# Performance work log

Measured on AMD Instinct MI355X. Metric: run time of the kernel, lower is better.

## Reference

```python
import jax, jax.numpy as jnp
import numpy as np
from jax import lax

B, S, N, C = 8, 256, 64, 64  # batch, time=freq (square, required by concat), n, c
EPS = 1e-3  # keras BatchNormalization / LayerNormalization default epsilon


def _conv(x, w, b):
    # 3x3 stride-1 SAME conv, NHWC / HWIO
    return lax.conv_general_dilated(x, w, (1, 1), 'SAME',
                                    dimension_numbers=('NHWC', 'HWIO', 'NHWC')) + b


def _bn(x, g, b):
    # training-mode batch norm: stats over batch+spatial axes
    m = jnp.mean(x, (0, 1, 2))
    v = jnp.var(x, (0, 1, 2))
    return (x - m) * lax.rsqrt(v + EPS) * g + b


def _ln(x, g, b):
    m = jnp.mean(x, -1, keepdims=True)
    v = jnp.var(x, -1, keepdims=True)
    return (x - m) * lax.rsqrt(v + EPS) * g + b


def _attn(q, k, v):
    # q,k,v: [B, C, L, D]; scaled dot-product attention over axis L
    d = q.shape[-1]
    s = jnp.einsum('bcid,bcjd->bcij', q, k) / jnp.sqrt(jnp.float32(d))
    a = jax.nn.softmax(s, axis=-1)
    return jnp.einsum('bcij,bcjd->bcid', a, v)


def setup_inputs():
    key = jax.random.key(0)
    ks = jax.random.split(key, 16)
    w = lambda k, sh: jax.random.normal(k, sh, jnp.float32) * 0.05
    inp = {
        'inputs': jax.random.normal(ks[0], (B, S, S, N), jnp.float32),
        'wq': w(ks[1], (3, 3, N, C)), 'bq': jnp.zeros((C,), jnp.float32),
        'wk': w(ks[2], (3, 3, N, C)), 'bk': jnp.zeros((C,), jnp.float32),
        'wv': w(ks[3], (3, 3, N, C)), 'bv': jnp.zeros((C,), jnp.float32),
        'gq': jnp.ones((C,), jnp.float32), 'betaq': jnp.zeros((C,), jnp.float32),
        'gk': jnp.ones((C,), jnp.float32), 'betak': jnp.zeros((C,), jnp.float32),
        'gv': jnp.ones((C,), jnp.float32), 'betav': jnp.zeros((C,), jnp.float32),
        'wc': w(ks[4], (3, 3, 2 * S, N)), 'bc': jnp.zeros((N,), jnp.float32),
        'ln_g': jnp.ones((N,), jnp.float32), 'ln_b': jnp.zeros((N,), jnp.float32),
        'w1': w(ks[5], (3, 3, N, N)), 'b1': jnp.zeros((N,), jnp.float32),
        'g1': jnp.ones((N,), jnp.float32), 'beta1': jnp.zeros((N,), jnp.float32),
        'w2': w(ks[6], (3, 3, N, N)), 'b2': jnp.zeros((N,), jnp.float32),
        'g2': jnp.ones((N,), jnp.float32), 'beta2': jnp.zeros((N,), jnp.float32),
    }
    return inp


def reference(inputs, wq, bq, wk, bk, wv, bv, gq, betaq, gk, betak, gv, betav,
              wc, bc, ln_g, ln_b, w1, b1, g1, beta1, w2, b2, g2, beta2):
    q = _bn(_conv(inputs, wq, bq), gq, betaq)
    k = _bn(_conv(inputs, wk, bk), gk, betak)
    v = _bn(_conv(inputs, wv, bv), gv, betav)
    # axial attention: over time ([B,C,T,F]) and over frequency ([B,C,F,T])
    qt, kt, vt = (jnp.transpose(t, (0, 3, 1, 2)) for t in (q, k, v))
    qf, kf, vf = (jnp.transpose(t, (0, 3, 2, 1)) for t in (q, k, v))
    at = _attn(qt, kt, vt)  # [B, C, S, S]
    af = _attn(qf, kf, vf)  # [B, C, S, S]
    out = jnp.concatenate([at, af], axis=-1)  # [B, C, S, 2S] treated as NHWC
    out = _ln(_conv(out, wc, bc), ln_g, ln_b)  # [B, C, S, N]
    f1 = _bn(jax.nn.relu(_conv(out, w1, b1)), g1, beta1)
    f2 = _bn(jax.nn.relu(_conv(f1, w2, b2)), g2, beta2)
    return f2
```

## Files before the change

### kernel.cpp

```cpp
#include <hip/hip_runtime.h>
#include <hip/hip_bf16.h>

typedef unsigned short u16;
typedef u16 us8 __attribute__((ext_vector_type(8)));
typedef u16 us4 __attribute__((ext_vector_type(4)));
typedef __bf16 bfx8 __attribute__((ext_vector_type(8)));
typedef float f32x4 __attribute__((ext_vector_type(4)));

#define EPS 1e-3f

__device__ __forceinline__ float bf2f(u16 u){ unsigned x = ((unsigned)u)<<16; return __builtin_bit_cast(float, x); }
__device__ __forceinline__ u16 f2bu(float f){ __hip_bfloat16 h = __float2bfloat16(f); return __builtin_bit_cast(u16, h); }
__device__ __forceinline__ bfx8 ldb8(const u16* p){ return __builtin_bit_cast(bfx8, *(const us8*)p); }

__global__ __launch_bounds__(256) void prepw_k(const float* __restrict__ src, u16* __restrict__ dst, int CI)
{
  int total = 9*CI*64;
  int idx = blockIdx.x*256 + threadIdx.x;
  if (idx < total){
    int ci = idx % CI; int rest = idx / CI; int co = rest & 63; int t = rest >> 6;
    dst[idx] = f2bu(src[((size_t)t*CI + ci)*64 + co]);
  }
}

__global__ __launch_bounds__(768) void conv_qkv_f32_k(
    const float* __restrict__ in,
    const u16* __restrict__ WtQ, const u16* __restrict__ WtK, const u16* __restrict__ WtV,
    const float* __restrict__ bq, const float* __restrict__ bk, const float* __restrict__ bv,
    u16* __restrict__ qo, u16* __restrict__ ko, u16* __restrict__ vo)
{
  int b = blockIdx.z, y0 = blockIdx.y*2, x0 = blockIdx.x*128;
  int tid = threadIdx.x, lane = tid & 63, wid = tid >> 6;
  int g3 = wid >> 2, wid4 = wid & 3;
  int l15 = lane & 15, lhi = lane >> 4;
  __shared__ u16 lds[4*130*64];

  for (int idx = tid; idx < 8320; idx += 768){
    int row = idx >> 4, c4 = idx & 15;
    int yy = row / 130, xx = row - yy*130;
    int gy = y0 + yy - 1, gx = x0 + xx - 1;
    us4 v = {0,0,0,0};
    if ((unsigned)gy < 256u && (unsigned)gx < 256u){
      float4 f = *(const float4*)(in + ((((size_t)b*256 + gy)*256 + gx)<<6) + c4*4);
      v[0] = f2bu(f.x); v[1] = f2bu(f.y); v[2] = f2bu(f.z); v[3] = f2bu(f.w);
    }
    *(us4*)(lds + row*64 + ((c4*4) ^ ((xx&7)<<3))) = v;
  }
  __syncthreads();

  const u16*  Wt   = (g3==0) ? WtQ : (g3==1) ? WtK : WtV;
  const float* bias = (g3==0) ? bq  : (g3==1) ? bk  : bv;
  u16*        outp = (g3==0) ? qo  : (g3==1) ? ko  : vo;

  f32x4 acc[2][2][4];
#pragma unroll
  for (int nf=0; nf<4; nf++){
    float bb = bias[nf*16 + l15];
#pragma unroll
    for (int ry=0; ry<2; ry++){
      acc[ry][0][nf] = (f32x4){bb,bb,bb,bb};
      acc[ry][1][nf] = (f32x4){bb,bb,bb,bb};
    }
  }
  int xbase = wid4*32;
#pragma unroll
  for (int ky=0; ky<3; ky++)
#pragma unroll
    for (int kx=0; kx<3; kx++){
      int t = ky*3 + kx;
      bfx8 bfr[2][4];
#pragma unroll
      for (int ks=0; ks<2; ks++)
#pragma unroll
        for (int nf=0; nf<4; nf++)
          bfr[ks][nf] = ldb8(Wt + ((t*64 + nf*16 + l15)<<6) + ks*32 + lhi*8);
#pragma unroll
      for (int ks=0; ks<2; ks++)
#pragma unroll
        for (int ry=0; ry<2; ry++)
#pragma unroll
          for (int mt=0; mt<2; mt++){
            int xx = xbase + mt*16 + l15 + kx;
            bfx8 a = ldb8(lds + ((ry+ky)*130 + xx)*64 + ((ks*32 + lhi*8) ^ ((xx&7)<<3)));
#pragma unroll
            for (int nf=0; nf<4; nf++)
              acc[ry][mt][nf] = __builtin_amdgcn_mfma_f32_16x16x32_bf16(a, bfr[ks][nf], acc[ry][mt][nf], 0,0,0);
          }
    }
#pragma unroll
  for (int ry=0; ry<2; ry++)
#pragma unroll
    for (int mt=0; mt<2; mt++)
#pragma unroll
      for (int nf=0; nf<4; nf++)
#pragma unroll
        for (int r=0; r<4; r++){
          int x = x0 + xbase + mt*16 + lhi*4 + r;
          outp[((((size_t)b*256 + (y0+ry))*256 + x)<<6) + nf*16 + l15] = f2bu(acc[ry][mt][nf][r]);
        }
}

template<bool RELU>
__global__ __launch_bounds__(256) void conv2_mfma_k(
    const u16* __restrict__ in, const u16* __restrict__ Wt, const float* __restrict__ bias,
    u16* __restrict__ out)
{
  int b = blockIdx.z, y0 = blockIdx.y*2, x0 = blockIdx.x*128;
  int tid = threadIdx.x, lane = tid & 63, wid = tid >> 6;
  int l15 = lane & 15, lhi = lane >> 4;
  __shared__ u16 lds[4*130*64];

  for (int idx = tid; idx < 4160; idx += 256){
    int row = idx >> 3, ch = idx & 7;
    int yy = row / 130, xx = row - yy*130;
    int gy = y0 + yy - 1, gx = x0 + xx - 1;
    us8 v = {0,0,0,0,0,0,0,0};
    if ((unsigned)gy < 64u && (unsigned)gx < 256u)
      v = *(const us8*)(in + ((((size_t)b*64 + gy)*256 + gx)<<6) + ch*8);
    *(us8*)(lds + row*64 + ((ch*8) ^ ((xx&7)<<3))) = v;
  }
  __syncthreads();

  f32x4 acc[2][2][4];
#pragma unroll
  for (int nf=0; nf<4; nf++){
    float bb = bias[nf*16 + l15];
#pragma unroll
    for (int ry=0; ry<2; ry++){
      acc[ry][0][nf] = (f32x4){bb,bb,bb,bb};
      acc[ry][1][nf] = (f32x4){bb,bb,bb,bb};
    }
  }
  int xbase = wid*32;
#pragma unroll
  for (int ky=0; ky<3; ky++)
#pragma unroll
    for (int kx=0; kx<3; kx++){
      int t = ky*3 + kx;
      bfx8 bfr[2][4];
#pragma unroll
      for (int ks=0; ks<2; ks++)
#pragma unroll
        for (int nf=0; nf<4; nf++)
          bfr[ks][nf] = ldb8(Wt + ((t*64 + nf*16 + l15)<<6) + ks*32 + lhi*8);
#pragma unroll
      for (int ks=0; ks<2; ks++)
#pragma unroll
        for (int ry=0; ry<2; ry++)
#pragma unroll
          for (int mt=0; mt<2; mt++){
            int xx = xbase + mt*16 + l15 + kx;
            bfx8 a = ldb8(lds + ((ry+ky)*130 + xx)*64 + ((ks*32 + lhi*8) ^ ((xx&7)<<3)));
#pragma unroll
            for (int nf=0; nf<4; nf++)
              acc[ry][mt][nf] = __builtin_amdgcn_mfma_f32_16x16x32_bf16(a, bfr[ks][nf], acc[ry][mt][nf], 0,0,0);
          }
    }
#pragma unroll
  for (int ry=0; ry<2; ry++)
#pragma unroll
    for (int mt=0; mt<2; mt++)
#pragma unroll
      for (int nf=0; nf<4; nf++)
#pragma unroll
        for (int r=0; r<4; r++){
          int x = x0 + xbase + mt*16 + lhi*4 + r;
          float vv = acc[ry][mt][nf][r];
          if (RELU) vv = fmaxf(vv, 0.f);
          out[((((size_t)b*64 + (y0+ry))*256 + x)<<6) + nf*16 + l15] = f2bu(vv);
        }
}

__global__ __launch_bounds__(256) void conv_cat_ln_k(
    const u16* __restrict__ in, const u16* __restrict__ Wt, const float* __restrict__ bias,
    const float* __restrict__ lng, const float* __restrict__ lnb, u16* __restrict__ out)
{
  int b = blockIdx.z, y0 = blockIdx.y*2, x0 = blockIdx.x*128;
  int tid = threadIdx.x, lane = tid & 63, wid = tid >> 6;
  int l15 = lane & 15, lhi = lane >> 4;
  __shared__ u16 lds[4*130*64];

  f32x4 acc[2][2][4];
#pragma unroll
  for (int nf=0; nf<4; nf++){
    float bb = bias[nf*16 + l15];
#pragma unroll
    for (int ry=0; ry<2; ry++){
      acc[ry][0][nf] = (f32x4){bb,bb,bb,bb};
      acc[ry][1][nf] = (f32x4){bb,bb,bb,bb};
    }
  }
  int xbase = wid*32;
  for (int ci0 = 0; ci0 < 512; ci0 += 64){
    __syncthreads();
    for (int idx = tid; idx < 4160; idx += 256){
      int row = idx >> 3, ch = idx & 7;
      int yy = row / 130, xx = row - yy*130;
      int gy = y0 + yy - 1, gx = x0 + xx - 1;
      us8 v = {0,0,0,0,0,0,0,0};
      if ((unsigned)gy < 64u && (unsigned)gx < 256u)
        v = *(const us8*)(in + ((((size_t)b*64 + gy)*256 + gx)<<9) + ci0 + ch*8);
      *(us8*)(lds + row*64 + ((ch*8) ^ ((xx&7)<<3))) = v;
    }
    __syncthreads();
#pragma unroll
    for (int ky=0; ky<3; ky++)
#pragma unroll
      for (int kx=0; kx<3; kx++){
        int t = ky*3 + kx;
        bfx8 bfr[2][4];
#pragma unroll
        for (int ks=0; ks<2; ks++)
#pragma unroll
          for (int nf=0; nf<4; nf++)
            bfr[ks][nf] = ldb8(Wt + ((size_t)(t*64 + nf*16 + l15)<<9) + ci0 + ks*32 + lhi*8);
#pragma unroll
        for (int ks=0; ks<2; ks++)
#pragma unroll
          for (int ry=0; ry<2; ry++)
#pragma unroll
            for (int mt=0; mt<2; mt++){
              int xx = xbase + mt*16 + l15 + kx;
              bfx8 a = ldb8(lds + ((ry+ky)*130 + xx)*64 + ((ks*32 + lhi*8) ^ ((xx&7)<<3)));
#pragma unroll
              for (int nf=0; nf<4; nf++)
                acc[ry][mt][nf] = __builtin_amdgcn_mfma_f32_16x16x32_bf16(a, bfr[ks][nf], acc[ry][mt][nf], 0,0,0);
            }
      }
  }
  float lg[4], lb[4];
#pragma unroll
  for (int nf=0; nf<4; nf++){ lg[nf] = lng[nf*16+l15]; lb[nf] = lnb[nf*16+l15]; }
#pragma unroll
  for (int ry=0; ry<2; ry++)
#pragma unroll
    for (int mt=0; mt<2; mt++)
#pragma unroll
      for (int r=0; r<4; r++){
        float v0 = acc[ry][mt][0][r], v1 = acc[ry][mt][1][r], v2 = acc[ry][mt][2][r], v3 = acc[ry][mt][3][r];
        float s = v0+v1+v2+v3;
        s += __shfl_xor(s,1); s += __shfl_xor(s,2); s += __shfl_xor(s,4); s += __shfl_xor(s,8);
        float m = s * 0.015625f;
        float d0=v0-m, d1=v1-m, d2=v2-m, d3=v3-m;
        float q = d0*d0+d1*d1+d2*d2+d3*d3;
        q += __shfl_xor(q,1); q += __shfl_xor(q,2); q += __shfl_xor(q,4); q += __shfl_xor(q,8);
        float rs = rsqrtf(q*0.015625f + EPS);
        int x = x0 + xbase + mt*16 + lhi*4 + r;
        size_t base = ((((size_t)b*64 + (y0+ry))*256 + x)<<6) + l15;
        out[base]    = f2bu(d0*rs*lg[0] + lb[0]);
        out[base+16] = f2bu(d1*rs*lg[1] + lb[1]);
        out[base+32] = f2bu(d2*rs*lg[2] + lb[2]);
        out[base+48] = f2bu(d3*rs*lg[3] + lb[3]);
      }
}

__global__ __launch_bounds__(256) void stats_k(const u16* __restrict__ x, size_t n4,
                                               float* __restrict__ partial)
{
  int tid = threadIdx.x;
  float s[4] = {0,0,0,0}, q[4] = {0,0,0,0};
  for (size_t i = (size_t)blockIdx.x*256 + tid; i < n4; i += (size_t)256*1024){
    us4 u = ((const us4*)x)[i];
#pragma unroll
    for (int e=0; e<4; e++){ float v = bf2f(u[e]); s[e] += v; q[e] += v*v; }
  }
  __shared__ float sm[256][8];
#pragma unroll
  for (int e=0; e<4; e++){ sm[tid][e] = s[e]; sm[tid][4+e] = q[e]; }
  __syncthreads();
  for (int st = 128; st >= 16; st >>= 1){
    if (tid < st)
#pragma unroll
      for (int e=0; e<8; e++) sm[tid][e] += sm[tid+st][e];
    __syncthreads();
  }
  if (tid < 16){
    int c0 = tid*4;
#pragma unroll
    for (int e=0; e<4; e++){
      partial[(size_t)blockIdx.x*128 + c0 + e]      = sm[tid][e];
      partial[(size_t)blockIdx.x*128 + 64 + c0 + e] = sm[tid][4+e];
    }
  }
}

__global__ __launch_bounds__(256) void finalize_k(const float* __restrict__ partial,
                                                  const float* __restrict__ g, const float* __restrict__ beta,
                                                  float inv_count, float* __restrict__ ss)
{
  __shared__ float sm[4][128];
  int c = threadIdx.x & 63, qq = threadIdx.x >> 6;
  float s = 0.f, v = 0.f;
  for (int i = qq*256; i < qq*256+256; i++){ s += partial[i*128 + c]; v += partial[i*128 + 64 + c]; }
  sm[qq][c] = s; sm[qq][64+c] = v;
  __syncthreads();
  if (qq == 0){
    s = sm[0][c]+sm[1][c]+sm[2][c]+sm[3][c];
    v = sm[0][64+c]+sm[1][64+c]+sm[2][64+c]+sm[3][64+c];
    float m = s*inv_count;
    float var = v*inv_count - m*m;
    float sc = g[c]*rsqrtf(var + EPS);
    ss[c] = sc; ss[64+c] = beta[c] - m*sc;
  }
}

__global__ __launch_bounds__(256) void bn_tr_k(const u16* __restrict__ x, const float* __restrict__ ss,
                                               u16* __restrict__ xT)
{
  int b = blockIdx.z, t = blockIdx.y, f0 = blockIdx.x*64;
  __shared__ float sm[64][65];
  int tid = threadIdx.x;
  for (int idx = tid; idx < 4096; idx += 256){
    int ci = idx & 63, fi = idx >> 6;
    float v = bf2f(x[((((size_t)b*256 + t)*256 + f0 + fi)<<6) + ci]);
    sm[fi][ci] = v*ss[ci] + ss[64+ci];
  }
  __syncthreads();
  for (int idx = tid; idx < 4096; idx += 256){
    int fi = idx & 63, ci = idx >> 6;
    xT[(((size_t)b*64 + ci)<<16) + t*256 + f0 + fi] = f2bu(sm[fi][ci]);
  }
}

template<bool TRA, bool TRB>
__global__ __launch_bounds__(256) void gemm_k(const u16* __restrict__ A, const u16* __restrict__ B,
                                              u16* __restrict__ C, float scale,
                                              int ldC, size_t cBatch, int cOff)
{
  int bc = blockIdx.z;
  const u16* Ab = A + ((size_t)bc<<16);
  const u16* Bb = B + ((size_t)bc<<16);
  u16* Cb = C + (size_t)bc*cBatch + cOff;
  int i0 = blockIdx.y*128, j0 = blockIdx.x*128;
  int tid = threadIdx.x, lane = tid & 63, wid = tid >> 6;
  int l15 = lane & 15, lhi = lane >> 4;
  __shared__ u16 Al[128*64], Bl[128*64];
  f32x4 acc[2][8] = {};

  for (int k0 = 0; k0 < 256; k0 += 64){
    __syncthreads();
    if (!TRA){
      for (int idx = tid; idx < 1024; idx += 256){
        int r = idx >> 3, c8 = idx & 7;
        us8 v = *(const us8*)(Ab + (size_t)(i0+r)*256 + k0 + c8*8);
        *(us8*)(Al + r*64 + ((c8*8) ^ ((r&7)<<3))) = v;
      }
    } else {
      for (int idx = tid; idx < 1024; idx += 256){
        int kr = idx >> 4, c8 = idx & 15;
        us8 v = *(const us8*)(Ab + (size_t)(k0+kr)*256 + i0 + c8*8);
#pragma unroll
        for (int e=0; e<8; e++){
          int i = c8*8 + e;
          Al[i*64 + (kr ^ ((i&7)<<3))] = v[e];
        }
      }
    }
    if (!TRB){
      for (int idx = tid; idx < 1024; idx += 256){
        int r = idx >> 3, c8 = idx & 7;
        us8 v = *(const us8*)(Bb + (size_t)(j0+r)*256 + k0 + c8*8);
        *(us8*)(Bl + r*64 + ((c8*8) ^ ((r&7)<<3))) = v;
      }
    } else {
      for (int idx = tid; idx < 1024; idx += 256){
        int kr = idx >> 4, c8 = idx & 15;
        us8 v = *(const us8*)(Bb + (size_t)(k0+kr)*256 + j0 + c8*8);
#pragma unroll
        for (int e=0; e<8; e++){
          int j = c8*8 + e;
          Bl[j*64 + (kr ^ ((j&7)<<3))] = v[e];
        }
      }
    }
    __syncthreads();
    int wrow = wid*32;
#pragma unroll
    for (int ks=0; ks<2; ks++){
      bfx8 bfr[8];
#pragma unroll
      for (int nf=0; nf<8; nf++)
        bfr[nf] = ldb8(Bl + (nf*16+l15)*64 + ((ks*32 + lhi*8) ^ ((l15&7)<<3)));
#pragma unroll
      for (int mt=0; mt<2; mt++){
        int r = wrow + mt*16 + l15;
        bfx8 a = ldb8(Al + r*64 + ((ks*32 + lhi*8) ^ ((r&7)<<3)));
#pragma unroll
        for (int nf=0; nf<8; nf++)
          acc[mt][nf] = __builtin_amdgcn_mfma_f32_16x16x32_bf16(a, bfr[nf], acc[mt][nf], 0,0,0);
      }
    }
  }
#pragma unroll
  for (int mt=0; mt<2; mt++)
#pragma unroll
    for (int nf=0; nf<8; nf++)
#pragma unroll
      for (int r=0; r<4; r++){
        int i = i0 + wid*32 + mt*16 + lhi*4 + r;
        int j = j0 + nf*16 + l15;
        Cb[(size_t)i*ldC + j] = f2bu(acc[mt][nf][r]*scale);
      }
}

__global__ __launch_bounds__(256) void softmax_k(u16* __restrict__ P)
{
  size_t row = (size_t)blockIdx.x*4 + (threadIdx.x >> 6);
  int lane = threadIdx.x & 63;
  u16* p = P + row*256 + lane*4;
  us4 u = *(us4*)p;
  float v[4];
#pragma unroll
  for (int e=0; e<4; e++) v[e] = bf2f(u[e]);
  float m = fmaxf(fmaxf(v[0],v[1]), fmaxf(v[2],v[3]));
  for (int off=1; off<64; off<<=1) m = fmaxf(m, __shfl_xor(m, off));
  float s = 0.f;
#pragma unroll
  for (int e=0; e<4; e++){ v[e] = __expf(v[e]-m); s += v[e]; }
  for (int off=1; off<64; off<<=1) s += __shfl_xor(s, off);
  float inv = 1.f/s;
  us4 o;
#pragma unroll
  for (int e=0; e<4; e++) o[e] = f2bu(v[e]*inv);
  *(us4*)p = o;
}

__global__ __launch_bounds__(256) void apply_bn_b_k(const u16* __restrict__ x, const float* __restrict__ ss,
                                                    u16* __restrict__ out, int n4)
{
  int i = blockIdx.x*256 + threadIdx.x;
  if (i < n4){
    int c0 = (i & 15)*4;
    us4 u = ((const us4*)x)[i];
    us4 o;
#pragma unroll
    for (int e=0; e<4; e++) o[e] = f2bu(bf2f(u[e])*ss[c0+e] + ss[64+c0+e]);
    ((us4*)out)[i] = o;
  }
}

__global__ __launch_bounds__(256) void apply_bn_f_k(const u16* __restrict__ x, const float* __restrict__ ss,
                                                    float* __restrict__ out, int n4)
{
  int i = blockIdx.x*256 + threadIdx.x;
  if (i < n4){
    int c0 = (i & 15)*4;
    us4 u = ((const us4*)x)[i];
    float4 o;
    o.x = bf2f(u[0])*ss[c0]   + ss[64+c0];
    o.y = bf2f(u[1])*ss[c0+1] + ss[64+c0+1];
    o.z = bf2f(u[2])*ss[c0+2] + ss[64+c0+2];
    o.w = bf2f(u[3])*ss[c0+3] + ss[64+c0+3];
    ((float4*)out)[i] = o;
  }
}

extern "C" void kernel_launch(void* const* d_in, const int* in_sizes, int n_in,
                              void* d_out, int out_size, void* d_ws, size_t ws_size,
                              hipStream_t stream)
{
  const float* in    = (const float*)d_in[0];
  const float* wq    = (const float*)d_in[1];  const float* bq    = (const float*)d_in[2];
  const float* wk    = (const float*)d_in[3];  const float* bk    = (const float*)d_in[4];
  const float* wv    = (const float*)d_in[5];  const float* bv    = (const float*)d_in[6];
  const float* gq    = (const float*)d_in[7];  const float* betaq = (const float*)d_in[8];
  const float* gk    = (const float*)d_in[9];  const float* betak = (const float*)d_in[10];
  const float* gv    = (const float*)d_in[11]; const float* betav = (const float*)d_in[12];
  const float* wc    = (const float*)d_in[13]; const float* bcv   = (const float*)d_in[14];
  const float* lng   = (const float*)d_in[15]; const float* lnb   = (const float*)d_in[16];
  const float* w1    = (const float*)d_in[17]; const float* b1    = (const float*)d_in[18];
  const float* g1    = (const float*)d_in[19]; const float* beta1 = (const float*)d_in[20];
  const float* w2    = (const float*)d_in[21]; const float* b2    = (const float*)d_in[22];
  const float* g2    = (const float*)d_in[23]; const float* beta2 = (const float*)d_in[24];
  float* out = (float*)d_out;

  char* ws = (char*)d_ws;
  const size_t MB = 1ull<<20;
  u16* qraw = (u16*)(ws);
  u16* kraw = (u16*)(ws + 64*MB);
  u16* vraw = (u16*)(ws + 128*MB);
  u16* qT   = (u16*)(ws + 192*MB);
  u16* kT   = (u16*)(ws + 256*MB);
  u16* vT   = (u16*)(ws + 320*MB);
  u16* P1   = qraw;
  u16* P2   = kraw;
  u16* cat  = qT;
  u16* y0   = (u16*)(ws + 128*MB);
  u16* f1   = (u16*)(ws + 144*MB);
  u16* rr   = (u16*)(ws + 160*MB);
  float* partial = (float*)(ws + 384*MB);
  float* ssq = (float*)(ws + 384*MB + 524288);
  float* ssk = ssq + 128;  float* ssv = ssq + 256;
  float* ss1 = ssq + 384;  float* ss2 = ssq + 512;
  u16* wqT = (u16*)(ws + 384*MB + 524288 + 4096);
  u16* wkT = wqT + 36864; u16* wvT = wkT + 36864;
  u16* w1T = wvT + 36864; u16* w2T = w1T + 36864;
  u16* wcT = w2T + 36864;

  dim3 blk(256);
  dim3 blk768(768);

  prepw_k<<<144, blk, 0, stream>>>(wq, wqT, 64);
  prepw_k<<<144, blk, 0, stream>>>(wk, wkT, 64);
  prepw_k<<<144, blk, 0, stream>>>(wv, wvT, 64);
  prepw_k<<<144, blk, 0, stream>>>(w1, w1T, 64);
  prepw_k<<<144, blk, 0, stream>>>(w2, w2T, 64);
  prepw_k<<<1152, blk, 0, stream>>>(wc, wcT, 512);

  const float invN1 = 1.f/524288.f;
  conv_qkv_f32_k<<<dim3(2,128,8), blk768, 0, stream>>>(in, wqT,wkT,wvT, bq,bk,bv, qraw,kraw,vraw);
  stats_k<<<1024, blk, 0, stream>>>(qraw, 8388608ull, partial);
  finalize_k<<<1, blk, 0, stream>>>(partial, gq, betaq, invN1, ssq);
  bn_tr_k<<<dim3(4,256,8), blk, 0, stream>>>(qraw, ssq, qT);
  stats_k<<<1024, blk, 0, stream>>>(kraw, 8388608ull, partial);
  finalize_k<<<1, blk, 0, stream>>>(partial, gk, betak, invN1, ssk);
  bn_tr_k<<<dim3(4,256,8), blk, 0, stream>>>(kraw, ssk, kT);
  stats_k<<<1024, blk, 0, stream>>>(vraw, 8388608ull, partial);
  finalize_k<<<1, blk, 0, stream>>>(partial, gv, betav, invN1, ssv);
  bn_tr_k<<<dim3(4,256,8), blk, 0, stream>>>(vraw, ssv, vT);

  gemm_k<false,false><<<dim3(2,2,512), blk, 0, stream>>>(qT, kT, P1, 0.0625f, 256, 65536, 0);
  gemm_k<true ,true ><<<dim3(2,2,512), blk, 0, stream>>>(qT, kT, P2, 0.0625f, 256, 65536, 0);
  softmax_k<<<65536, blk, 0, stream>>>(P1);
  gemm_k<false,true ><<<dim3(2,2,512), blk, 0, stream>>>(P1, vT, cat, 1.f, 512, 131072, 0);
  gemm_k<false,false><<<dim3(2,2,512), blk, 0, stream>>>(P2, vT, cat, 1.f, 512, 131072, 256);

  conv_cat_ln_k<<<dim3(2,32,8), blk, 0, stream>>>(cat, wcT, bcv, lng, lnb, y0);

  const float invN2 = 1.f/131072.f;
  conv2_mfma_k<true><<<dim3(2,32,8), blk, 0, stream>>>(y0, w1T, b1, rr);
  stats_k<<<1024, blk, 0, stream>>>(rr, 2097152ull, partial);
  finalize_k<<<1, blk, 0, stream>>>(partial, g1, beta1, invN2, ss1);
  apply_bn_b_k<<<8192, blk, 0, stream>>>(rr, ss1, f1, 2097152);

  conv2_mfma_k<true><<<dim3(2,32,8), blk, 0, stream>>>(f1, w2T, b2, rr);
  stats_k<<<1024, blk, 0, stream>>>(rr, 2097152ull, partial);
  finalize_k<<<1, blk, 0, stream>>>(partial, g2, beta2, invN2, ss2);
  apply_bn_f_k<<<8192, blk, 0, stream>>>(rr, ss2, out, 2097152);
}
```

Measured before the change: 1.249 ms.

## Prefetch conv weights, vectorize BN transpose, shrink stats grid

The three MFMA conv kernels now double-buffer weight fragments in registers, loading the next tap's weights while the current tap's MFMAs run, which hides global load latency. The bn_tr kernel switches to 8-wide vector loads and stores for both reading and the transposed write. The stats reduction drops from 1024 to 256 blocks, and finalize is adjusted to match, which cuts the partial-sum traffic and the final reduce work. The register prefetch raises register pressure and could lower occupancy.

```diff
diff --git a/kernel.cpp b/kernel.cpp
--- a/kernel.cpp
+++ b/kernel.cpp
@@ -63,30 +63,45 @@
     }
   }
   int xbase = wid4*32;
-#pragma unroll
-  for (int ky=0; ky<3; ky++)
-#pragma unroll
-    for (int kx=0; kx<3; kx++){
-      int t = ky*3 + kx;
-      bfx8 bfr[2][4];
+
+  bfx8 bw[2][4];
+#pragma unroll
+  for (int ks=0; ks<2; ks++)
+#pragma unroll
+    for (int nf=0; nf<4; nf++)
+      bw[ks][nf] = ldb8(Wt + ((nf*16 + l15)<<6) + ks*32 + lhi*8);
+
+#pragma unroll
+  for (int t=0; t<9; t++){
+    bfx8 bwn[2][4];
+    if (t < 8){
 #pragma unroll
       for (int ks=0; ks<2; ks++)
 #pragma unroll
         for (int nf=0; nf<4; nf++)
-          bfr[ks][nf] = ldb8(Wt + ((t*64 + nf*16 + l15)<<6) + ks*32 + lhi*8);
+          bwn[ks][nf] = ldb8(Wt + (((t+1)*64 + nf*16 + l15)<<6) + ks*32 + lhi*8);
+    }
+    int ky = t/3, kx = t - ky*3;
+#pragma unroll
+    for (int ks=0; ks<2; ks++)
+#pragma unroll
+      for (int ry=0; ry<2; ry++)
+#pragma unroll
+        for (int mt=0; mt<2; mt++){
+          int xx = xbase + mt*16 + l15 + kx;
+          bfx8 a = ldb8(lds + ((ry+ky)*130 + xx)*64 + ((ks*32 + lhi*8) ^ ((xx&7)<<3)));
+#pragma unroll
+          for (int nf=0; nf<4; nf++)
+            acc[ry][mt][nf] = __builtin_amdgcn_mfma_f32_16x16x32_bf16(a, bw[ks][nf], acc[ry][mt][nf], 0,0,0);
+        }
+    if (t < 8){
 #pragma unroll
       for (int ks=0; ks<2; ks++)
 #pragma unroll
-        for (int ry=0; ry<2; ry++)
-#pragma unroll
-          for (int mt=0; mt<2; mt++){
-            int xx = xbase + mt*16 + l15 + kx;
-            bfx8 a = ldb8(lds + ((ry+ky)*130 + xx)*64 + ((ks*32 + lhi*8) ^ ((xx&7)<<3)));
-#pragma unroll
-            for (int nf=0; nf<4; nf++)
-              acc[ry][mt][nf] = __builtin_amdgcn_mfma_f32_16x16x32_bf16(a, bfr[ks][nf], acc[ry][mt][nf], 0,0,0);
-          }
-    }
+        for (int nf=0; nf<4; nf++)
+          bw[ks][nf] = bwn[ks][nf];
+    }
+  }
 #pragma unroll
   for (int ry=0; ry<2; ry++)
 #pragma unroll
@@ -132,30 +147,45 @@
     }
   }
   int xbase = wid*32;
-#pragma unroll
-  for (int ky=0; ky<3; ky++)
-#pragma unroll
-    for (int kx=0; kx<3; kx++){
-      int t = ky*3 + kx;
-      bfx8 bfr[2][4];
+
+  bfx8 bw[2][4];
+#pragma unroll
+  for (int ks=0; ks<2; ks++)
+#pragma unroll
+    for (int nf=0; nf<4; nf++)
+      bw[ks][nf] = ldb8(Wt + ((nf*16 + l15)<<6) + ks*32 + lhi*8);
+
+#pragma unroll
+  for (int t=0; t<9; t++){
+    bfx8 bwn[2][4];
+    if (t < 8){
 #pragma unroll
       for (int ks=0; ks<2; ks++)
 #pragma unroll
         for (int nf=0; nf<4; nf++)
-          bfr[ks][nf] = ldb8(Wt + ((t*64 + nf*16 + l15)<<6) + ks*32 + lhi*8);
+          bwn[ks][nf] = ldb8(Wt + (((t+1)*64 + nf*16 + l15)<<6) + ks*32 + lhi*8);
+    }
+    int ky = t/3, kx = t - ky*3;
+#pragma unroll
+    for (int ks=0; ks<2; ks++)
+#pragma unroll
+      for (int ry=0; ry<2; ry++)
+#pragma unroll
+        for (int mt=0; mt<2; mt++){
+          int xx = xbase + mt*16 + l15 + kx;
+          bfx8 a = ldb8(lds + ((ry+ky)*130 + xx)*64 + ((ks*32 + lhi*8) ^ ((xx&7)<<3)));
+#pragma unroll
+          for (int nf=0; nf<4; nf++)
+            acc[ry][mt][nf] = __builtin_amdgcn_mfma_f32_16x16x32_bf16(a, bw[ks][nf], acc[ry][mt][nf], 0,0,0);
+        }
+    if (t < 8){
 #pragma unroll
       for (int ks=0; ks<2; ks++)
 #pragma unroll
-        for (int ry=0; ry<2; ry++)
-#pragma unroll
-          for (int mt=0; mt<2; mt++){
-            int xx = xbase + mt*16 + l15 + kx;
-            bfx8 a = ldb8(lds + ((ry+ky)*130 + xx)*64 + ((ks*32 + lhi*8) ^ ((xx&7)<<3)));
-#pragma unroll
-            for (int nf=0; nf<4; nf++)
-              acc[ry][mt][nf] = __builtin_amdgcn_mfma_f32_16x16x32_bf16(a, bfr[ks][nf], acc[ry][mt][nf], 0,0,0);
-          }
-    }
+        for (int nf=0; nf<4; nf++)
+          bw[ks][nf] = bwn[ks][nf];
+    }
+  }
 #pragma unroll
   for (int ry=0; ry<2; ry++)
 #pragma unroll
@@ -203,30 +233,45 @@
       *(us8*)(lds + row*64 + ((ch*8) ^ ((xx&7)<<3))) = v;
     }
     __syncthreads();
-#pragma unroll
-    for (int ky=0; ky<3; ky++)
-#pragma unroll
-      for (int kx=0; kx<3; kx++){
-        int t = ky*3 + kx;
-        bfx8 bfr[2][4];
+
+    bfx8 bw[2][4];
+#pragma unroll
+    for (int ks=0; ks<2; ks++)
+#pragma unroll
+      for (int nf=0; nf<4; nf++)
+        bw[ks][nf] = ldb8(Wt + ((size_t)(nf*16 + l15)<<9) + ci0 + ks*32 + lhi*8);
+
+#pragma unroll
+    for (int t=0; t<9; t++){
+      bfx8 bwn[2][4];
+      if (t < 8){
 #pragma unroll
         for (int ks=0; ks<2; ks++)
 #pragma unroll
           for (int nf=0; nf<4; nf++)
-            bfr[ks][nf] = ldb8(Wt + ((size_t)(t*64 + nf*16 + l15)<<9) + ci0 + ks*32 + lhi*8);
+            bwn[ks][nf] = ldb8(Wt + ((size_t)((t+1)*64 + nf*16 + l15)<<9) + ci0 + ks*32 + lhi*8);
+      }
+      int ky = t/3, kx = t - ky*3;
+#pragma unroll
+      for (int ks=0; ks<2; ks++)
+#pragma unroll
+        for (int ry=0; ry<2; ry++)
+#pragma unroll
+          for (int mt=0; mt<2; mt++){
+            int xx = xbase + mt*16 + l15 + kx;
+            bfx8 a = ldb8(lds + ((ry+ky)*130 + xx)*64 + ((ks*32 + lhi*8) ^ ((xx&7)<<3)));
+#pragma unroll
+            for (int nf=0; nf<4; nf++)
+              acc[ry][mt][nf] = __builtin_amdgcn_mfma_f32_16x16x32_bf16(a, bw[ks][nf], acc[ry][mt][nf], 0,0,0);
+          }
+      if (t < 8){
 #pragma unroll
         for (int ks=0; ks<2; ks++)
 #pragma unroll
-          for (int ry=0; ry<2; ry++)
-#pragma unroll
-            for (int mt=0; mt<2; mt++){
-              int xx = xbase + mt*16 + l15 + kx;
-              bfx8 a = ldb8(lds + ((ry+ky)*130 + xx)*64 + ((ks*32 + lhi*8) ^ ((xx&7)<<3)));
-#pragma unroll
-              for (int nf=0; nf<4; nf++)
-                acc[ry][mt][nf] = __builtin_amdgcn_mfma_f32_16x16x32_bf16(a, bfr[ks][nf], acc[ry][mt][nf], 0,0,0);
-            }
-      }
+          for (int nf=0; nf<4; nf++)
+            bw[ks][nf] = bwn[ks][nf];
+      }
+    }
   }
   float lg[4], lb[4];
 #pragma unroll
@@ -259,7 +304,7 @@
 {
   int tid = threadIdx.x;
   float s[4] = {0,0,0,0}, q[4] = {0,0,0,0};
-  for (size_t i = (size_t)blockIdx.x*256 + tid; i < n4; i += (size_t)256*1024){
+  for (size_t i = (size_t)blockIdx.x*256 + tid; i < n4; i += (size_t)256*256){
     us4 u = ((const us4*)x)[i];
 #pragma unroll
     for (int e=0; e<4; e++){ float v = bf2f(u[e]); s[e] += v; q[e] += v*v; }
@@ -291,7 +336,7 @@
   __shared__ float sm[4][128];
   int c = threadIdx.x & 63, qq = threadIdx.x >> 6;
   float s = 0.f, v = 0.f;
-  for (int i = qq*256; i < qq*256+256; i++){ s += partial[i*128 + c]; v += partial[i*128 + 64 + c]; }
+  for (int i = qq*64; i < qq*64+64; i++){ s += partial[i*128 + c]; v += partial[i*128 + 64 + c]; }
   sm[qq][c] = s; sm[qq][64+c] = v;
   __syncthreads();
   if (qq == 0){
@@ -310,15 +355,22 @@
   int b = blockIdx.z, t = blockIdx.y, f0 = blockIdx.x*64;
   __shared__ float sm[64][65];
   int tid = threadIdx.x;
-  for (int idx = tid; idx < 4096; idx += 256){
-    int ci = idx & 63, fi = idx >> 6;
-    float v = bf2f(x[((((size_t)b*256 + t)*256 + f0 + fi)<<6) + ci]);
-    sm[fi][ci] = v*ss[ci] + ss[64+ci];
+  for (int idx = tid; idx < 512; idx += 256){
+    int fi = idx >> 3, cg = idx & 7;
+    us8 v = *(const us8*)(x + ((((size_t)b*256 + t)*256 + f0 + fi)<<6) + cg*8);
+#pragma unroll
+    for (int e=0; e<8; e++){
+      int ci = cg*8 + e;
+      sm[fi][ci] = bf2f(v[e])*ss[ci] + ss[64+ci];
+    }
   }
   __syncthreads();
-  for (int idx = tid; idx < 4096; idx += 256){
-    int fi = idx & 63, ci = idx >> 6;
-    xT[(((size_t)b*64 + ci)<<16) + t*256 + f0 + fi] = f2bu(sm[fi][ci]);
+  for (int idx = tid; idx < 512; idx += 256){
+    int ci = idx >> 3, fg = idx & 7;
+    us8 o;
+#pragma unroll
+    for (int e=0; e<8; e++) o[e] = f2bu(sm[fg*8+e][ci]);
+    *(us8*)(xT + (((size_t)b*64 + ci)<<16) + t*256 + f0 + fg*8) = o;
   }
 }
 
@@ -509,13 +561,13 @@
 
   const float invN1 = 1.f/524288.f;
   conv_qkv_f32_k<<<dim3(2,128,8), blk768, 0, stream>>>(in, wqT,wkT,wvT, bq,bk,bv, qraw,kraw,vraw);
-  stats_k<<<1024, blk, 0, stream>>>(qraw, 8388608ull, partial);
+  stats_k<<<256, blk, 0, stream>>>(qraw, 8388608ull, partial);
   finalize_k<<<1, blk, 0, stream>>>(partial, gq, betaq, invN1, ssq);
   bn_tr_k<<<dim3(4,256,8), blk, 0, stream>>>(qraw, ssq, qT);
-  stats_k<<<1024, blk, 0, stream>>>(kraw, 8388608ull, partial);
+  stats_k<<<256, blk, 0, stream>>>(kraw, 8388608ull, partial);
   finalize_k<<<1, blk, 0, stream>>>(partial, gk, betak, invN1, ssk);
   bn_tr_k<<<dim3(4,256,8), blk, 0, stream>>>(kraw, ssk, kT);
-  stats_k<<<1024, blk, 0, stream>>>(vraw, 8388608ull, partial);
+  stats_k<<<256, blk, 0, stream>>>(vraw, 8388608ull, partial);
   finalize_k<<<1, blk, 0, stream>>>(partial, gv, betav, invN1, ssv);
   bn_tr_k<<<dim3(4,256,8), blk, 0, stream>>>(vraw, ssv, vT);
 
@@ -529,12 +581,12 @@
 
   const float invN2 = 1.f/131072.f;
   conv2_mfma_k<true><<<dim3(2,32,8), blk, 0, stream>>>(y0, w1T, b1, rr);
-  stats_k<<<1024, blk, 0, stream>>>(rr, 2097152ull, partial);
+  stats_k<<<256, blk, 0, stream>>>(rr, 2097152ull, partial);
   finalize_k<<<1, blk, 0, stream>>>(partial, g1, beta1, invN2, ss1);
   apply_bn_b_k<<<8192, blk, 0, stream>>>(rr, ss1, f1, 2097152);
 
   conv2_mfma_k<true><<<dim3(2,32,8), blk, 0, stream>>>(f1, w2T, b2, rr);
-  stats_k<<<1024, blk, 0, stream>>>(rr, 2097152ull, partial);
+  stats_k<<<256, blk, 0, stream>>>(rr, 2097152ull, partial);
   finalize_k<<<1, blk, 0, stream>>>(partial, g2, beta2, invN2, ss2);
   apply_bn_f_k<<<8192, blk, 0, stream>>>(rr, ss2, out, 2097152);
 }
```

Result: slower. 1.417 ms (+13.5%).
